# Optimization experiments

Hardware: AMD Instinct MI355X
Metric: run time of the kernel (lower is better)

Reference implementation:

```python
import jax, jax.numpy as jnp
import numpy as np

GRID = 25
NUM_NODE = GRID * GRID  # 625, hard-coded by the original module

def _neighbor_flat_indices():
    # Replicates the torch index construction exactly, incl. boundary shifts.
    offsets = np.array([[-1,-1],[-1,0],[-1,1],[0,-1],[0,0],[0,1],[1,-1],[1,0],[1,1]])
    idx = np.arange(NUM_NODE)
    rows = idx // GRID
    cols = idx % GRID
    nr = rows[:, None] + offsets[:, 0]   # [625, 9]
    nc = cols[:, None] + offsets[:, 1]
    nr = nr.reshape(GRID, GRID, 9)
    nr[0, :, :] += 1                     # reflect top boundary
    nr[-1, :, :] -= 1                    # reflect bottom boundary
    nr = nr.reshape(NUM_NODE, 9)
    nc = nc.reshape(GRID, GRID, 9)
    nc[:, 0, :] += 1                     # reflect left boundary
    nc[:, -1, :] -= 1                    # reflect right boundary
    nc = nc.reshape(NUM_NODE, 9)
    return jnp.asarray(nr * GRID + nc)   # [625, 9] flat node indices

NEIGH = _neighbor_flat_indices()

def setup_inputs() -> dict:
    key = jax.random.key(0)
    k1, k2, k3, k4, k5 = jax.random.split(key, 5)
    B = 512
    x = jax.random.normal(k1, (B, NUM_NODE, 66), dtype=jnp.float32)
    # nn.Linear(66, 64): weight [64, 66], bias [64]
    W_fc = jax.random.normal(k2, (64, 66), dtype=jnp.float32) * (1.0 / np.sqrt(66))
    b_fc = jax.random.normal(k3, (64,), dtype=jnp.float32) * 0.01
    # nn.Linear(128, 1): weight [1, 128], bias [1]
    W_at = jax.random.normal(k4, (1, 128), dtype=jnp.float32) * (1.0 / np.sqrt(128))
    b_at = jax.random.normal(k5, (1,), dtype=jnp.float32) * 0.01
    return {"x": x, "W_fc": W_fc, "b_fc": b_fc, "W_at": W_at, "b_at": b_at}

def reference(x, W_fc, b_fc, W_at, b_at):
    # h = fc(x): [B, 625, 64]
    h = jnp.einsum('bnf,df->bnd', x, W_fc) + b_fc
    # Gather fixed 9-neighbor features: [B, 625, 9, 64]
    x2 = h[:, NEIGH, :]
    # Center feature broadcast to the 9 neighbor slots: [B, 625, 9, 64]
    x1 = jnp.broadcast_to(h[:, :, None, :], x2.shape)
    z = jnp.concatenate([x1, x2], axis=-1)                  # [B, 625, 9, 128]
    s = jnp.einsum('bnkf,of->bnko', z, W_at) + b_at          # [B, 625, 9, 1]
    s = jax.nn.leaky_relu(s, negative_slope=0.01)[..., 0]    # [B, 625, 9]
    # exp(s) / sum(exp(s)) over the 9 neighbors == softmax(s)
    attn_weight = jax.nn.softmax(s, axis=-1)                 # [B, 625, 9]
    # Original: sum_k h[:, :, None, :] * w[..., None] over k
    # = h * sum_k w  (h does not depend on k); avoids a [B,625,9,64] temp.
    attn_vector = h * jnp.sum(attn_weight, axis=-1, keepdims=True)  # [B, 625, 64]
    return (attn_vector, attn_weight)
```

## Files before the change

### kernel.cpp

```cpp
#include <hip/hip_runtime.h>

#define BATCH 512
#define GRID_N 25
#define NODES 625
#define BN (BATCH * NODES)
#define NTILES (BN / 16)
#define F 66
#define D 64
#define TILE_FLOATS (16 * F)
#define WPB 4
#define TPW 2
#define NBLOCKS (NTILES / (WPB * TPW))

typedef short bf16x8 __attribute__((ext_vector_type(8)));
typedef float f32x4  __attribute__((ext_vector_type(4)));

__device__ __forceinline__ short f2bf(float f) {
    union { float f; unsigned u; } c; c.f = f;
    unsigned r = c.u + 0x7fffu + ((c.u >> 16) & 1u);
    return (short)(r >> 16);
}

__device__ __forceinline__ void stage16(const float* g, float* l) {
    __builtin_amdgcn_global_load_lds(
        (const __attribute__((address_space(1))) float*)g,
        (__attribute__((address_space(3))) float*)l,
        16, 0, 0);
}

__global__ __launch_bounds__(256, 4) void fc_mfma(
    const float* __restrict__ x, const float* __restrict__ Wfc,
    const float* __restrict__ bfc, const float* __restrict__ Wat,
    float* __restrict__ hout, float* __restrict__ u, float* __restrict__ v)
{
    const int tid  = threadIdx.x;
    const int lane = tid & 63;
    const int wid  = tid >> 6;
    const int l15  = lane & 15;
    const int quad = lane >> 4;
    const int gw   = blockIdx.x * WPB + wid;

    __shared__ float smem[WPB * TPW * TILE_FLOATS];
    float* sbuf = smem + wid * (TPW * TILE_FLOATS);

    const int tile0 = gw * TPW;

#pragma unroll
    for (int t = 0; t < TPW; ++t) {
        const float* g = x + (size_t)(tile0 + t) * TILE_FLOATS;
        float* s = sbuf + t * TILE_FLOATS;
#pragma unroll
        for (int i = 0; i < 4; ++i)
            stage16(g + i * 256 + lane * 4, s + i * 256 + lane * 4);
        if (lane < 8)
            stage16(g + 1024 + lane * 4, s + 1024 + lane * 4);
    }

    bf16x8 bfrag[4][3];
#pragma unroll
    for (int t = 0; t < 4; ++t) {
        const float* wr = Wfc + (t * 16 + l15) * F;
#pragma unroll
        for (int c = 0; c < 2; ++c) {
            bf16x8 fr;
#pragma unroll
            for (int j = 0; j < 8; ++j) fr[j] = f2bf(wr[c * 32 + quad * 8 + j]);
            bfrag[t][c] = fr;
        }
        bf16x8 z = {0, 0, 0, 0, 0, 0, 0, 0};
        if (quad == 0) { z[0] = f2bf(wr[64]); z[1] = f2bf(wr[65]); }
        bfrag[t][2] = z;
    }
    float bft[4], wa1[4], wa2[4];
#pragma unroll
    for (int t = 0; t < 4; ++t) {
        bft[t] = bfc[t * 16 + l15];
        wa1[t] = Wat[t * 16 + l15];
        wa2[t] = Wat[64 + t * 16 + l15];
    }

    __builtin_amdgcn_s_waitcnt(0x0F70);
    asm volatile("" ::: "memory");

#pragma unroll
    for (int t = 0; t < TPW; ++t) {
        const int bn0 = (tile0 + t) * 16;
        const float2* row = (const float2*)(sbuf + t * TILE_FLOATS) + l15 * (F / 2);

        float xv[16];
#pragma unroll
        for (int c = 0; c < 2; ++c)
#pragma unroll
            for (int j2 = 0; j2 < 4; ++j2) {
                const float2 p = row[c * 16 + quad * 4 + j2];
                xv[c * 8 + j2 * 2]     = p.x;
                xv[c * 8 + j2 * 2 + 1] = p.y;
            }
        bf16x8 afrag[3];
#pragma unroll
        for (int c = 0; c < 2; ++c) {
            bf16x8 fr;
#pragma unroll
            for (int j = 0; j < 8; ++j) fr[j] = f2bf(xv[c * 8 + j]);
            afrag[c] = fr;
        }
        {
            bf16x8 z = {0, 0, 0, 0, 0, 0, 0, 0};
            if (quad == 0) {
                const float2 p = row[32];
                z[0] = f2bf(p.x); z[1] = f2bf(p.y);
            }
            afrag[2] = z;
        }

        f32x4 acc[4] = {{0,0,0,0},{0,0,0,0},{0,0,0,0},{0,0,0,0}};
#pragma unroll
        for (int nt = 0; nt < 4; ++nt)
#pragma unroll
            for (int c = 0; c < 3; ++c)
                acc[nt] = __builtin_amdgcn_mfma_f32_16x16x32_bf16(afrag[c], bfrag[nt][c], acc[nt], 0, 0, 0);

        float pu[4] = {0, 0, 0, 0}, pv[4] = {0, 0, 0, 0};
#pragma unroll
        for (int nt = 0; nt < 4; ++nt) {
#pragma unroll
            for (int r = 0; r < 4; ++r) {
                const float h = acc[nt][r] + bft[nt];
                hout[(size_t)(bn0 + quad * 4 + r) * D + nt * 16 + l15] = h;
                pu[r] = fmaf(h, wa1[nt], pu[r]);
                pv[r] = fmaf(h, wa2[nt], pv[r]);
            }
        }
#pragma unroll
        for (int off = 8; off > 0; off >>= 1) {
#pragma unroll
            for (int r = 0; r < 4; ++r) {
                pu[r] += __shfl_xor(pu[r], off, 64);
                pv[r] += __shfl_xor(pv[r], off, 64);
            }
        }
        if (l15 == 0) {
#pragma unroll
            for (int r = 0; r < 4; ++r) {
                u[bn0 + quad * 4 + r] = pu[r];
                v[bn0 + quad * 4 + r] = pv[r];
            }
        }
    }
}

__global__ __launch_bounds__(256) void attn_kernel(
    const float* __restrict__ u, const float* __restrict__ v,
    const float* __restrict__ bat, float* __restrict__ wout)
{
    const int bn = blockIdx.x * blockDim.x + threadIdx.x;
    if (bn >= BN) return;

    const int b   = bn / NODES;
    const int n   = bn - b * NODES;
    const int row = n / GRID_N;
    const int col = n - row * GRID_N;
    const int r0 = row + (row == 0) - (row == GRID_N - 1);
    const int c0 = col + (col == 0) - (col == GRID_N - 1);

    const float* vb = v + b * NODES;
    const float u0 = u[bn] + bat[0];

    float s[9];
#pragma unroll
    for (int k = 0; k < 9; ++k) {
        const int nr = r0 + (k / 3) - 1;
        const int nc = c0 + (k % 3) - 1;
        const float t = u0 + vb[nr * GRID_N + nc];
        s[k] = (t >= 0.0f) ? t : 0.01f * t;
    }
    float m = s[0];
#pragma unroll
    for (int k = 1; k < 9; ++k) m = fmaxf(m, s[k]);
    float sum = 0.0f;
#pragma unroll
    for (int k = 0; k < 9; ++k) { s[k] = __expf(s[k] - m); sum += s[k]; }
    const float inv = 1.0f / sum;
#pragma unroll
    for (int k = 0; k < 9; ++k) wout[(size_t)bn * 9 + k] = s[k] * inv;
}

extern "C" void kernel_launch(void* const* d_in, const int* in_sizes, int n_in,
                              void* d_out, int out_size, void* d_ws, size_t ws_size,
                              hipStream_t stream)
{
    const float* x   = (const float*)d_in[0];
    const float* Wfc = (const float*)d_in[1];
    const float* bfc = (const float*)d_in[2];
    const float* Wat = (const float*)d_in[3];
    const float* bat = (const float*)d_in[4];

    float* hout = (float*)d_out;
    float* wout = (float*)d_out + (size_t)BN * D;
    float* u = (float*)d_ws;
    float* v = u + BN;

    fc_mfma<<<NBLOCKS, 256, 0, stream>>>(x, Wfc, bfc, Wat, hout, u, v);
    attn_kernel<<<(BN + 255) / 256, 256, 0, stream>>>(u, v, bat, wout);
}
```

Measured before the change: 190.5 us.

## Load x directly into registers and stage outputs through LDS for coalesced stores

```diff
diff --git a/kernel.cpp b/kernel.cpp
--- a/kernel.cpp
+++ b/kernel.cpp
@@ -7,7 +7,6 @@
 #define NTILES (BN / 16)
 #define F 66
 #define D 64
-#define TILE_FLOATS (16 * F)
 #define WPB 4
 #define TPW 2
 #define NBLOCKS (NTILES / (WPB * TPW))
@@ -21,14 +20,7 @@
     return (short)(r >> 16);
 }
 
-__device__ __forceinline__ void stage16(const float* g, float* l) {
-    __builtin_amdgcn_global_load_lds(
-        (const __attribute__((address_space(1))) float*)g,
-        (__attribute__((address_space(3))) float*)l,
-        16, 0, 0);
-}
-
-__global__ __launch_bounds__(256, 4) void fc_mfma(
+__global__ __launch_bounds__(256, 3) void fc_mfma(
     const float* __restrict__ x, const float* __restrict__ Wfc,
     const float* __restrict__ bfc, const float* __restrict__ Wat,
     float* __restrict__ hout, float* __restrict__ u, float* __restrict__ v)
@@ -39,36 +31,42 @@
     const int l15  = lane & 15;
     const int quad = lane >> 4;
     const int gw   = blockIdx.x * WPB + wid;
-
-    __shared__ float smem[WPB * TPW * TILE_FLOATS];
-    float* sbuf = smem + wid * (TPW * TILE_FLOATS);
-
     const int tile0 = gw * TPW;
 
+    __shared__ float smem[WPB * 256 * 4];
+    float* tbuf = smem + wid * 1024;
+
+    float2 xb[TPW][9];
 #pragma unroll
     for (int t = 0; t < TPW; ++t) {
-        const float* g = x + (size_t)(tile0 + t) * TILE_FLOATS;
-        float* s = sbuf + t * TILE_FLOATS;
-#pragma unroll
-        for (int i = 0; i < 4; ++i)
-            stage16(g + i * 256 + lane * 4, s + i * 256 + lane * 4);
-        if (lane < 8)
-            stage16(g + 1024 + lane * 4, s + 1024 + lane * 4);
+        const float2* rp = (const float2*)x + (size_t)(tile0 + t) * 528 + l15 * 33;
+#pragma unroll
+        for (int j2 = 0; j2 < 4; ++j2) xb[t][j2]     = rp[quad * 4 + j2];
+#pragma unroll
+        for (int j2 = 0; j2 < 4; ++j2) xb[t][4 + j2] = rp[16 + quad * 4 + j2];
+        if (quad == 0) xb[t][8] = rp[32];
     }
 
     bf16x8 bfrag[4][3];
 #pragma unroll
     for (int t = 0; t < 4; ++t) {
-        const float* wr = Wfc + (t * 16 + l15) * F;
+        const float2* wr = (const float2*)Wfc + (t * 16 + l15) * 33;
 #pragma unroll
         for (int c = 0; c < 2; ++c) {
             bf16x8 fr;
 #pragma unroll
-            for (int j = 0; j < 8; ++j) fr[j] = f2bf(wr[c * 32 + quad * 8 + j]);
+            for (int j2 = 0; j2 < 4; ++j2) {
+                const float2 p = wr[c * 16 + quad * 4 + j2];
+                fr[j2 * 2]     = f2bf(p.x);
+                fr[j2 * 2 + 1] = f2bf(p.y);
+            }
             bfrag[t][c] = fr;
         }
         bf16x8 z = {0, 0, 0, 0, 0, 0, 0, 0};
-        if (quad == 0) { z[0] = f2bf(wr[64]); z[1] = f2bf(wr[65]); }
+        if (quad == 0) {
+            const float2 p = wr[32];
+            z[0] = f2bf(p.x); z[1] = f2bf(p.y);
+        }
         bfrag[t][2] = z;
     }
     float bft[4], wa1[4], wa2[4];
@@ -79,37 +77,25 @@
         wa2[t] = Wat[64 + t * 16 + l15];
     }
 
-    __builtin_amdgcn_s_waitcnt(0x0F70);
-    asm volatile("" ::: "memory");
-
 #pragma unroll
     for (int t = 0; t < TPW; ++t) {
         const int bn0 = (tile0 + t) * 16;
-        const float2* row = (const float2*)(sbuf + t * TILE_FLOATS) + l15 * (F / 2);
-
-        float xv[16];
-#pragma unroll
-        for (int c = 0; c < 2; ++c)
-#pragma unroll
-            for (int j2 = 0; j2 < 4; ++j2) {
-                const float2 p = row[c * 16 + quad * 4 + j2];
-                xv[c * 8 + j2 * 2]     = p.x;
-                xv[c * 8 + j2 * 2 + 1] = p.y;
-            }
+
         bf16x8 afrag[3];
 #pragma unroll
         for (int c = 0; c < 2; ++c) {
             bf16x8 fr;
 #pragma unroll
-            for (int j = 0; j < 8; ++j) fr[j] = f2bf(xv[c * 8 + j]);
+            for (int j2 = 0; j2 < 4; ++j2) {
+                const float2 p = xb[t][c * 4 + j2];
+                fr[j2 * 2]     = f2bf(p.x);
+                fr[j2 * 2 + 1] = f2bf(p.y);
+            }
             afrag[c] = fr;
         }
         {
             bf16x8 z = {0, 0, 0, 0, 0, 0, 0, 0};
-            if (quad == 0) {
-                const float2 p = row[32];
-                z[0] = f2bf(p.x); z[1] = f2bf(p.y);
-            }
+            if (quad == 0) { z[0] = f2bf(xb[t][8].x); z[1] = f2bf(xb[t][8].y); }
             afrag[2] = z;
         }
 
@@ -126,7 +112,7 @@
 #pragma unroll
             for (int r = 0; r < 4; ++r) {
                 const float h = acc[nt][r] + bft[nt];
-                hout[(size_t)(bn0 + quad * 4 + r) * D + nt * 16 + l15] = h;
+                tbuf[(quad * 4 + r) * 64 + nt * 16 + l15] = h;
                 pu[r] = fmaf(h, wa1[nt], pu[r]);
                 pv[r] = fmaf(h, wa2[nt], pv[r]);
             }
@@ -146,6 +132,11 @@
                 v[bn0 + quad * 4 + r] = pv[r];
             }
         }
+        float4* dst = (float4*)(hout + (size_t)bn0 * D);
+        const float4* src = (const float4*)tbuf;
+#pragma unroll
+        for (int i = 0; i < 4; ++i)
+            dst[i * 64 + lane] = src[i * 64 + lane];
     }
 }
 
@@ -153,8 +144,11 @@
     const float* __restrict__ u, const float* __restrict__ v,
     const float* __restrict__ bat, float* __restrict__ wout)
 {
-    const int bn = blockIdx.x * blockDim.x + threadIdx.x;
-    if (bn >= BN) return;
+    __shared__ float sw[256 * 9];
+    const int tid  = threadIdx.x;
+    const int lane = tid & 63;
+    const int wid  = tid >> 6;
+    const int bn   = blockIdx.x * 256 + tid;
 
     const int b   = bn / NODES;
     const int n   = bn - b * NODES;
@@ -181,8 +175,16 @@
 #pragma unroll
     for (int k = 0; k < 9; ++k) { s[k] = __expf(s[k] - m); sum += s[k]; }
     const float inv = 1.0f / sum;
-#pragma unroll
-    for (int k = 0; k < 9; ++k) wout[(size_t)bn * 9 + k] = s[k] * inv;
+
+    float* ws = sw + wid * 576;
+#pragma unroll
+    for (int k = 0; k < 9; ++k) ws[lane * 9 + k] = s[k] * inv;
+
+    float4* dst = (float4*)(wout + (size_t)(blockIdx.x * 256 + wid * 64) * 9);
+    const float4* src = (const float4*)ws;
+    dst[lane]      = src[lane];
+    dst[64 + lane] = src[64 + lane];
+    if (lane < 16) dst[128 + lane] = src[128 + lane];
 }
 
 extern "C" void kernel_launch(void* const* d_in, const int* in_sizes, int n_in,
@@ -201,5 +203,5 @@
     float* v = u + BN;
 
     fc_mfma<<<NBLOCKS, 256, 0, stream>>>(x, Wfc, bfc, Wat, hout, u, v);
-    attn_kernel<<<(BN + 255) / 256, 256, 0, stream>>>(u, v, bat, wout);
-}
+    attn_kernel<<<BN / 256, 256, 0, stream>>>(u, v, bat, wout);
+}
```

New measurement: 176.0 us. 1.08x faster.
